# Optimization experiments

Measured on AMD Instinct MI355X. Metric: run time of the kernel, lower is better.

## Reference

```python
import jax, jax.numpy as jnp
import numpy as np

B, E, T, N = 1024, 512, 8, 256


def setup_inputs() -> dict:
    key = jax.random.key(0)
    k1, k2, k3, k4 = jax.random.split(key, 4)
    weights = jax.random.uniform(k1, (T,), dtype=jnp.float32)  # one scalar per bond type
    bond_src = jax.random.randint(k2, (B, E), 0, N - 1, dtype=jnp.int32)  # raw i, offset +1 later
    bond_dst = jax.random.randint(k3, (B, E), 0, N - 1, dtype=jnp.int32)
    bond_type = jax.random.randint(k4, (B, E), 0, T, dtype=jnp.int32)
    return {"weights": weights, "bond_src": bond_src, "bond_dst": bond_dst,
            "bond_type": bond_type, "num_nodes": N}


def reference(weights, bond_src, bond_dst, bond_type, num_nodes):
    # Gather per-bond weight, then symmetric scatter into dense [B, N, N] adjacency.
    batch, n_edges = bond_src.shape
    w = weights[bond_type]                                  # [B, E] gather
    bidx = jnp.broadcast_to(jnp.arange(batch)[:, None], (batch, n_edges))
    src = bond_src + 1                                      # +1 node offset as in torch code
    dst = bond_dst + 1
    bond_matrix = jnp.zeros((batch, num_nodes, num_nodes), dtype=weights.dtype)
    bond_matrix = bond_matrix.at[bidx, src, dst].set(w)
    bond_matrix = bond_matrix.at[bidx, dst, src].set(w)
    return bond_matrix
```

## Files before the change

### kernel.cpp

```cpp
#include <hip/hip_runtime.h>


#define NB_E 512
#define NB_N 256
#define CH_ROWS 32
#define SEQ_WORDS (CH_ROWS * NB_N / 2)
#define W_FLOATS  (CH_ROWS * NB_N)

typedef float v4f __attribute__((ext_vector_type(4)));

__device__ __forceinline__ void lds_max_u16(unsigned int* tab, int cell, unsigned int v16)
{
    unsigned int* w = tab + (cell >> 1);
    const int sh = (cell & 1) * 16;
    unsigned int old = *w;
    while (true) {
        const unsigned int cur = (old >> sh) & 0xFFFFu;
        if (cur >= v16) break;
        const unsigned int nw = (old & ~(0xFFFFu << sh)) | (v16 << sh);
        const unsigned int seen = atomicCAS(w, old, nw);
        if (seen == old) break;
        old = seen;
    }
}

__global__ __launch_bounds__(256) void BondWeight_41738492182540_kernel(
    const float* __restrict__ weights,
    const int*   __restrict__ bsrc,
    const int*   __restrict__ bdst,
    const int*   __restrict__ btyp,
    float*       __restrict__ out)
{
    __shared__ unsigned int seqtab[SEQ_WORDS];
    __shared__ float        wtab[W_FLOATS];

    const int bx = blockIdx.x;
    const int b  = bx >> 3;
    const int r0 = (bx & 7) * CH_ROWS;
    const int t  = threadIdx.x;

    {
        uint4* s4 = (uint4*)seqtab;
        #pragma unroll
        for (int k = 0; k < SEQ_WORDS / 4 / 256; ++k)
            s4[t + 256 * k] = make_uint4(0u, 0u, 0u, 0u);
        float4* w4 = (float4*)wtab;
        const float4 fz = make_float4(0.f, 0.f, 0.f, 0.f);
        #pragma unroll
        for (int k = 0; k < W_FLOATS / 4 / 256; ++k)
            w4[t + 256 * k] = fz;
    }

    const int2 s2 = ((const int2*)(bsrc + b * NB_E))[t];
    const int2 d2 = ((const int2*)(bdst + b * NB_E))[t];
    const int2 y2 = ((const int2*)(btyp + b * NB_E))[t];
    const float wA = weights[y2.x & 7];
    const float wB = weights[y2.y & 7];

    int cell[4]; unsigned int pk[4]; float wv[4]; bool inw[4];
    {
        const int e0 = 2 * t, e1 = 2 * t + 1;
        const int sa = s2.x + 1, da = d2.x + 1;
        const int sb = s2.y + 1, db = d2.y + 1;
        const unsigned int ta = (unsigned int)y2.x & 7u;
        const unsigned int tb = (unsigned int)y2.y & 7u;
        const int rr[4] = { sa, sb, da, db };
        const int cc[4] = { da, db, sa, sb };
        const unsigned int qq[4] = {
            ((unsigned int)(e0 + 1) << 3) | ta,
            ((unsigned int)(e1 + 1) << 3) | tb,
            ((unsigned int)(NB_E + e0 + 1) << 3) | ta,
            ((unsigned int)(NB_E + e1 + 1) << 3) | tb };
        const float ww[4] = { wA, wB, wA, wB };
        #pragma unroll
        for (int i = 0; i < 4; ++i) {
            const int r = rr[i] - r0;
            inw[i]  = (0 <= r) && (r < CH_ROWS);
            cell[i] = r * NB_N + cc[i];
            pk[i]   = qq[i];
            wv[i]   = ww[i];
        }
    }

    __syncthreads();

    #pragma unroll
    for (int i = 0; i < 4; ++i)
        if (inw[i]) lds_max_u16(seqtab, cell[i], pk[i]);

    __syncthreads();

    #pragma unroll
    for (int i = 0; i < 4; ++i) {
        if (inw[i]) {
            const unsigned int w32 = seqtab[cell[i] >> 1];
            const unsigned int cur = (w32 >> ((cell[i] & 1) * 16)) & 0xFFFFu;
            if (cur == pk[i]) wtab[cell[i]] = wv[i];
        }
    }

    __syncthreads();

    v4f* __restrict__ out4 = ((v4f*)out)
        + (size_t)b * (NB_N * NB_N / 4) + r0 * (NB_N / 4);
    const v4f* __restrict__ w4 = (const v4f*)wtab;

    #pragma unroll
    for (int k = 0; k < W_FLOATS / 4 / 256; ++k) {
        const int i4 = t + 256 * k;
        out4[i4] = w4[i4];
    }
}

extern "C" void kernel_launch(void* const* d_in, const int* in_sizes, int n_in,
                              void* d_out, int out_size, void* d_ws, size_t ws_size,
                              hipStream_t stream) {
    const float* weights = (const float*)d_in[0];
    const int*   bsrc    = (const int*)d_in[1];
    const int*   bdst    = (const int*)d_in[2];
    const int*   btyp    = (const int*)d_in[3];
    float*       out     = (float*)d_out;

    const int nb = in_sizes[1] / NB_E;

    BondWeight_41738492182540_kernel<<<nb * 8, 256, 0, stream>>>(
        weights, bsrc, bdst, btyp, out);
}
```

Baseline: 279.9 us.

## Split into global zero-fill kernel plus sparse scatter kernel with larger row chunks

Replaces the single kernel, which staged each row chunk in LDS and streamed it out, with two kernels. A grid-stride kernel zero-fills the whole output, then a scatter kernel writes only the winning cells straight to global memory. The chunk height doubles to 64 rows, so each block loads its batch's edges half as often. The cost is a second launch, scattered uncoalesced global stores, and an ordering dependency between the two kernels on the stream.

After: 303.4 us. +8.4%, slower.

```diff
diff --git a/kernel.cpp b/kernel.cpp
--- a/kernel.cpp
+++ b/kernel.cpp
@@ -3,11 +3,16 @@
 
 #define NB_E 512
 #define NB_N 256
-#define CH_ROWS 32
+#define CH_ROWS 64
 #define SEQ_WORDS (CH_ROWS * NB_N / 2)
-#define W_FLOATS  (CH_ROWS * NB_N)
 
-typedef float v4f __attribute__((ext_vector_type(4)));
+__global__ __launch_bounds__(256) void bw_zero_fill(
+    float4* __restrict__ o, int n4)
+{
+    const float4 z = make_float4(0.f, 0.f, 0.f, 0.f);
+    for (int i = blockIdx.x * 256 + threadIdx.x; i < n4; i += gridDim.x * 256)
+        o[i] = z;
+}
 
 __device__ __forceinline__ void lds_max_u16(unsigned int* tab, int cell, unsigned int v16)
 {
@@ -24,7 +29,7 @@
     }
 }
 
-__global__ __launch_bounds__(256) void BondWeight_41738492182540_kernel(
+__global__ __launch_bounds__(256) void bw_scatter(
     const float* __restrict__ weights,
     const int*   __restrict__ bsrc,
     const int*   __restrict__ bdst,
@@ -32,11 +37,10 @@
     float*       __restrict__ out)
 {
     __shared__ unsigned int seqtab[SEQ_WORDS];
-    __shared__ float        wtab[W_FLOATS];
 
     const int bx = blockIdx.x;
-    const int b  = bx >> 3;
-    const int r0 = (bx & 7) * CH_ROWS;
+    const int b  = bx >> 2;
+    const int r0 = (bx & 3) * CH_ROWS;
     const int t  = threadIdx.x;
 
     {
@@ -44,11 +48,6 @@
         #pragma unroll
         for (int k = 0; k < SEQ_WORDS / 4 / 256; ++k)
             s4[t + 256 * k] = make_uint4(0u, 0u, 0u, 0u);
-        float4* w4 = (float4*)wtab;
-        const float4 fz = make_float4(0.f, 0.f, 0.f, 0.f);
-        #pragma unroll
-        for (int k = 0; k < W_FLOATS / 4 / 256; ++k)
-            w4[t + 256 * k] = fz;
     }
 
     const int2 s2 = ((const int2*)(bsrc + b * NB_E))[t];
@@ -90,25 +89,14 @@
 
     __syncthreads();
 
+    float* __restrict__ tile = out + (size_t)b * (NB_N * NB_N) + r0 * NB_N;
     #pragma unroll
     for (int i = 0; i < 4; ++i) {
         if (inw[i]) {
             const unsigned int w32 = seqtab[cell[i] >> 1];
             const unsigned int cur = (w32 >> ((cell[i] & 1) * 16)) & 0xFFFFu;
-            if (cur == pk[i]) wtab[cell[i]] = wv[i];
+            if (cur == pk[i]) tile[cell[i]] = wv[i];
         }
-    }
-
-    __syncthreads();
-
-    v4f* __restrict__ out4 = ((v4f*)out)
-        + (size_t)b * (NB_N * NB_N / 4) + r0 * (NB_N / 4);
-    const v4f* __restrict__ w4 = (const v4f*)wtab;
-
-    #pragma unroll
-    for (int k = 0; k < W_FLOATS / 4 / 256; ++k) {
-        const int i4 = t + 256 * k;
-        out4[i4] = w4[i4];
     }
 }
 
@@ -122,7 +110,8 @@
     float*       out     = (float*)d_out;
 
     const int nb = in_sizes[1] / NB_E;
+    const int n4 = (nb * NB_N * NB_N) / 4;
 
-    BondWeight_41738492182540_kernel<<<nb * 8, 256, 0, stream>>>(
-        weights, bsrc, bdst, btyp, out);
+    bw_zero_fill<<<4096, 256, 0, stream>>>((float4*)out, n4);
+    bw_scatter<<<nb * 4, 256, 0, stream>>>(weights, bsrc, bdst, btyp, out);
 }
```
